# Optimization experiments

Hardware: AMD Instinct MI355X
Metric: run time of the kernel (lower is better)

The kernel has to match this reference:

```python
import jax, jax.numpy as jnp
import numpy as np

WS = 7  # window_size


def setup_inputs() -> dict:
    key = jax.random.key(0)
    ks = jax.random.split(key, 4)
    B, C, H, W = 4, 384, 56, 56
    NH = 12
    x = jax.random.normal(ks[0], (B, C, H, W), dtype=jnp.float32)
    # 1x1 conv weights act as per-pixel linear maps over channels
    w_qkv = jax.random.normal(ks[1], (3 * C, C), dtype=jnp.float32) * (C ** -0.5)
    b_qkv = jnp.zeros((3 * C,), dtype=jnp.float32)
    w_proj = jax.random.normal(ks[2], (C, C), dtype=jnp.float32) * (C ** -0.5)
    b_proj = jnp.zeros((C,), dtype=jnp.float32)
    rel_bias = jax.random.normal(ks[3], (NH, WS, WS), dtype=jnp.float32) * 0.02
    return {"x": x, "w_qkv": w_qkv, "b_qkv": b_qkv,
            "w_proj": w_proj, "b_proj": b_proj, "rel_bias": rel_bias}


def reference(x, w_qkv, b_qkv, w_proj, b_proj, rel_bias):
    # Neighborhood attention: each query (i,j) attends to a ws x ws window of
    # keys/values centered at (i,j); borders handled by replication padding
    # (ReplicationPad2d), with a learned relative position bias (nh, ws, ws).
    B, C, H, W = x.shape
    nh, ws, _ = rel_bias.shape
    hd = C // nh
    p = ws // 2
    scale = hd ** -0.5

    # qkv 1x1 conv -> (B, 3, nh, hd, H, W)
    qkv = jnp.einsum('oc,bchw->bohw', w_qkv, x) + b_qkv[None, :, None, None]
    qkv = qkv.reshape(B, 3, nh, hd, H, W)
    q, k, v = qkv[:, 0] * scale, qkv[:, 1], qkv[:, 2]

    pad = ((0, 0), (0, 0), (0, 0), (p, p), (p, p))
    k_pad = jnp.pad(k, pad, mode='edge')  # replication padding
    v_pad = jnp.pad(v, pad, mode='edge')

    # attention logits over the ws*ws window offsets: (B, nh, H, W, K)
    logits = jnp.stack(
        [jnp.einsum('bnchw,bnchw->bnhw', q, k_pad[..., di:di + H, dj:dj + W])
         for di in range(ws) for dj in range(ws)], axis=-1)
    logits = logits + rel_bias.reshape(nh, ws * ws)[None, :, None, None, :]
    attn = jax.nn.softmax(logits, axis=-1)  # (attn_drop is identity in eval)

    # value windows: (B, nh, K, hd, H, W)
    v_win = jnp.stack([v_pad[..., di:di + H, dj:dj + W]
                       for di in range(ws) for dj in range(ws)], axis=2)
    out = jnp.einsum('bnhwk,bnkchw->bnchw', attn, v_win).reshape(B, C, H, W)

    # output projection 1x1 conv (proj_drop is identity in eval)
    out = jnp.einsum('oc,bchw->bohw', w_proj, out) + b_proj[None, :, None, None]
    return out
```

## Files before the change

### kernel.cpp

```cpp
#include <hip/hip_runtime.h>
#include <hip/hip_bf16.h>
#include <hip/hip_fp16.h>

#define S_HW 3136
#define SP   3200
#define IMG_W 56
#define C_DIM 384
#define NH_DIM 12
#define QKV_C 1152
#define F16_ROWS 768

#define TB 16
#define HALO 22
#define NPX 484
#define PLANE_B 3880

typedef float f32x4 __attribute__((ext_vector_type(4)));
typedef float f32x2 __attribute__((ext_vector_type(2)));
typedef short bf16x8 __attribute__((ext_vector_type(8)));
typedef _Float16 f16x2 __attribute__((ext_vector_type(2)));

__device__ __forceinline__ void gld_lds16(const void* g, void* lds) {
    __builtin_amdgcn_global_load_lds(
        (const __attribute__((address_space(1))) void*)g,
        (__attribute__((address_space(3))) void*)lds, 16, 0, 0);
}

__device__ __forceinline__ float u2f(unsigned int u) { return __uint_as_float(u); }
__device__ __forceinline__ unsigned int f2bf_bits(float f) {
    unsigned int u = __float_as_uint(f);
    u += 0x7FFF + ((u >> 16) & 1);
    return u >> 16;
}
__device__ __forceinline__ unsigned int f2h_bits(float f) {
    return (unsigned int)__half_as_ushort(__float2half(f));
}

__global__ __launch_bounds__(256) void convert_w2_kernel(
    const float* __restrict__ a, int na, __hip_bfloat16* __restrict__ oa,
    const float* __restrict__ b, int nb, __hip_bfloat16* __restrict__ ob)
{
    int i = blockIdx.x * 256 + threadIdx.x;
    if (i < na) oa[i] = __float2bfloat16(a[i]);
    else if (i < na + nb) ob[i - na] = __float2bfloat16(b[i - na]);
}

__global__ __launch_bounds__(256) void transpose_convert_kernel(
    const float* __restrict__ x, __hip_bfloat16* __restrict__ xt)
{
    __shared__ float t[32][33];
    const int b = blockIdx.z;
    const int c0 = blockIdx.y * 32, s0 = blockIdx.x * 32;
    const int tid = threadIdx.x;

    const int lc = tid >> 3, ls = (tid & 7) * 4;
    float4 v = *reinterpret_cast<const float4*>(
        &x[((size_t)b * C_DIM + c0 + lc) * S_HW + s0 + ls]);
    t[lc][ls + 0] = v.x; t[lc][ls + 1] = v.y;
    t[lc][ls + 2] = v.z; t[lc][ls + 3] = v.w;
    __syncthreads();

    const int ws = tid >> 3, wc = (tid & 7) * 4;
    uint2 pk;
    pk.x = f2bf_bits(t[wc + 0][ws]) | (f2bf_bits(t[wc + 1][ws]) << 16);
    pk.y = f2bf_bits(t[wc + 2][ws]) | (f2bf_bits(t[wc + 3][ws]) << 16);
    *reinterpret_cast<uint2*>(
        &xt[((size_t)b * SP + s0 + ws) * C_DIM + c0 + wc]) = pk;
}

template <bool TRANS_OUT, typename OutT>
__global__ __launch_bounds__(256) void gemm_bf16_mfma(
    const __hip_bfloat16* __restrict__ A,
    const __hip_bfloat16* __restrict__ Bt,
    const float* __restrict__ bias,
    OutT* __restrict__ Y,
    int O, int K, float qscale, int qrows, int f16rows)
{
    __shared__ char smem[16384];
    char* As = smem;
    char* Bs = smem + 8192;

    const int b   = blockIdx.z;
    const int m0  = blockIdx.y * 128;
    const int n0  = blockIdx.x * 128;
    const int tid = threadIdx.x;
    const int w = tid >> 6, l = tid & 63;
    const int wr = w >> 1, wc = w & 1;

    const int srow = l >> 2;
    const int skk  = (l & 3) * 8;

    const __hip_bfloat16* Bb = Bt + (size_t)b * SP * K;

    f32x4 acc[4][4];
    #pragma unroll
    for (int i = 0; i < 4; ++i)
        #pragma unroll
        for (int j = 0; j < 4; ++j) {
            f32x4 z = {0.f, 0.f, 0.f, 0.f};
            acc[i][j] = z;
        }

    const int frow = l & 15;
    const int fk   = (l >> 4) * 16;

    for (int k0 = 0; k0 < K; k0 += 32) {
        #pragma unroll
        for (int j = 0; j < 2; ++j) {
            const int chunk = w * 2 + j;
            const int m = chunk * 16 + srow;
            gld_lds16(A  + (size_t)(m0 + m) * K + k0 + skk, As + chunk * 1024);
            gld_lds16(Bb + (size_t)(n0 + m) * K + k0 + skk, Bs + chunk * 1024);
        }
        __syncthreads();
        bf16x8 af[4], bfr[4];
        #pragma unroll
        for (int mi = 0; mi < 4; ++mi)
            af[mi] = *reinterpret_cast<const bf16x8*>(
                As + (wr * 64 + mi * 16 + frow) * 64 + fk);
        #pragma unroll
        for (int ni = 0; ni < 4; ++ni)
            bfr[ni] = *reinterpret_cast<const bf16x8*>(
                Bs + (wc * 64 + ni * 16 + frow) * 64 + fk);
        #pragma unroll
        for (int mi = 0; mi < 4; ++mi)
            #pragma unroll
            for (int ni = 0; ni < 4; ++ni)
                acc[mi][ni] = __builtin_amdgcn_mfma_f32_16x16x32_bf16(
                    af[mi], bfr[ni], acc[mi][ni], 0, 0, 0);
        __syncthreads();
    }

    const int crow0 = (l >> 4) * 4;
    const int ccol  = l & 15;
    if (TRANS_OUT) {
        __hip_bfloat16* Yb = (__hip_bfloat16*)Y + (size_t)b * SP * O;
        #pragma unroll
        for (int ni = 0; ni < 4; ++ni) {
            const int col = n0 + wc * 64 + ni * 16 + ccol;
            if (col >= S_HW) continue;
            #pragma unroll
            for (int mi = 0; mi < 4; ++mi) {
                const int row0 = m0 + wr * 64 + mi * 16 + crow0;
                const float sc = (row0 < qrows) ? qscale : 1.f;
                float v0 = (acc[mi][ni][0] + bias[row0 + 0]) * sc;
                float v1 = (acc[mi][ni][1] + bias[row0 + 1]) * sc;
                float v2 = (acc[mi][ni][2] + bias[row0 + 2]) * sc;
                float v3 = (acc[mi][ni][3] + bias[row0 + 3]) * sc;
                uint2 pk;
                if (row0 < f16rows) {
                    pk.x = f2h_bits(v0) | (f2h_bits(v1) << 16);
                    pk.y = f2h_bits(v2) | (f2h_bits(v3) << 16);
                } else {
                    pk.x = f2bf_bits(v0) | (f2bf_bits(v1) << 16);
                    pk.y = f2bf_bits(v2) | (f2bf_bits(v3) << 16);
                }
                *reinterpret_cast<uint2*>(&Yb[(size_t)col * O + row0]) = pk;
            }
        }
    } else {
        float* Yb = (float*)Y + (size_t)b * O * S_HW;
        #pragma unroll
        for (int ni = 0; ni < 4; ++ni) {
            const int col = n0 + wc * 64 + ni * 16 + ccol;
            if (col >= S_HW) continue;
            #pragma unroll
            for (int mi = 0; mi < 4; ++mi) {
                #pragma unroll
                for (int r = 0; r < 4; ++r) {
                    const int row = m0 + wr * 64 + mi * 16 + crow0 + r;
                    float v = acc[mi][ni][r] + bias[row];
                    if (row < qrows) v *= qscale;
                    Yb[(size_t)row * S_HW + col] = v;
                }
            }
        }
    }
}

__global__ __launch_bounds__(256, 4) void na_attn_kernel(
    const __hip_bfloat16* __restrict__ qkvt, const float* __restrict__ rel_bias,
    __hip_bfloat16* __restrict__ outt)
{
    __shared__ alignas(16) char halo[8 * PLANE_B];

    const int blk  = blockIdx.x;
    const int tile = blk & 15;
    const int bn   = blk >> 4;
    const int nh   = bn % NH_DIM;
    const int b    = bn / NH_DIM;
    const int th0  = (tile >> 2) * TB;
    const int tw0  = (tile & 3) * TB;

    const int tid = threadIdx.x;
    const int ty = tid >> 4, tx = tid & 15;
    const int h = th0 + ty, w = tw0 + tx;
    const bool valid = (h < 56) && (w < 56);
    const int s = h * IMG_W + w;

    const __hip_bfloat16* base = qkvt + (size_t)b * SP * QKV_C;
    const int co = nh * 32;

    #pragma unroll
    for (int i = 0; i < 8; ++i) {
        const int idx = tid + i * 256;
        if (idx < NPX * 4) {
            const int px = idx >> 2, g = idx & 3;
            const int hy = px / HALO, hx = px - hy * HALO;
            const int y = min(max(th0 - 3 + hy, 0), 55);
            const int x = min(max(tw0 - 3 + hx, 0), 55);
            const uint4 v = *reinterpret_cast<const uint4*>(
                base + (size_t)(y * IMG_W + x) * QKV_C + C_DIM + co + g * 8);
            uint2 lo; lo.x = v.x; lo.y = v.y;
            uint2 hi; hi.x = v.z; hi.y = v.w;
            *reinterpret_cast<uint2*>(&halo[(2 * g + 0) * PLANE_B + px * 8]) = lo;
            *reinterpret_cast<uint2*>(&halo[(2 * g + 1) * PLANE_B + px * 8]) = hi;
        }
    }

    unsigned int qreg[16];
    if (valid) {
        const uint4* qp = reinterpret_cast<const uint4*>(base + (size_t)s * QKV_C + co);
        #pragma unroll
        for (int g = 0; g < 4; ++g) {
            uint4 qg = qp[g];
            qreg[4 * g + 0] = qg.x; qreg[4 * g + 1] = qg.y;
            qreg[4 * g + 2] = qg.z; qreg[4 * g + 3] = qg.w;
        }
    }
    __syncthreads();

    float logits[49];
    if (valid) {
        #pragma unroll
        for (int di = 0; di < 7; ++di) {
            #pragma unroll
            for (int dj = 0; dj < 7; ++dj) {
                const int hp = (ty + di) * HALO + (tx + dj);
                const char* hb = halo + hp * 8;
                float acc0 = 0.f, acc1 = 0.f;
                #pragma unroll
                for (int pl = 0; pl < 8; ++pl) {
                    uint2 kk = *reinterpret_cast<const uint2*>(hb + pl * PLANE_B);
#if __has_builtin(__builtin_amdgcn_fdot2)
                    acc0 = __builtin_amdgcn_fdot2(
                        __builtin_bit_cast(f16x2, qreg[2 * pl]),
                        __builtin_bit_cast(f16x2, kk.x), acc0, false);
                    acc1 = __builtin_amdgcn_fdot2(
                        __builtin_bit_cast(f16x2, qreg[2 * pl + 1]),
                        __builtin_bit_cast(f16x2, kk.y), acc1, false);
#else
                    f16x2 qa = __builtin_bit_cast(f16x2, qreg[2 * pl]);
                    f16x2 qb = __builtin_bit_cast(f16x2, qreg[2 * pl + 1]);
                    f16x2 ka = __builtin_bit_cast(f16x2, kk.x);
                    f16x2 kb = __builtin_bit_cast(f16x2, kk.y);
                    acc0 += (float)qa[0] * (float)ka[0] + (float)qa[1] * (float)ka[1];
                    acc1 += (float)qb[0] * (float)kb[0] + (float)qb[1] * (float)kb[1];
#endif
                }
                logits[di * 7 + dj] = acc0 + acc1 + rel_bias[(nh * 7 + di) * 7 + dj];
            }
        }
    }
    __syncthreads();

    #pragma unroll
    for (int i = 0; i < 8; ++i) {
        const int idx = tid + i * 256;
        if (idx < NPX * 4) {
            const int px = idx >> 2, g = idx & 3;
            const int hy = px / HALO, hx = px - hy * HALO;
            const int y = min(max(th0 - 3 + hy, 0), 55);
            const int x = min(max(tw0 - 3 + hx, 0), 55);
            const uint4 v = *reinterpret_cast<const uint4*>(
                base + (size_t)(y * IMG_W + x) * QKV_C + 2 * C_DIM + co + g * 8);
            uint2 lo; lo.x = v.x; lo.y = v.y;
            uint2 hi; hi.x = v.z; hi.y = v.w;
            *reinterpret_cast<uint2*>(&halo[(2 * g + 0) * PLANE_B + px * 8]) = lo;
            *reinterpret_cast<uint2*>(&halo[(2 * g + 1) * PLANE_B + px * 8]) = hi;
        }
    }

    unsigned int ppk[25];
    float inv = 0.f;
    if (valid) {
        float mx = logits[0];
        #pragma unroll
        for (int i = 1; i < 49; ++i) mx = fmaxf(mx, logits[i]);
        float sum = 0.f;
        #pragma unroll
        for (int i = 0; i < 24; ++i) {
            float e0 = __expf(logits[2 * i] - mx);
            float e1 = __expf(logits[2 * i + 1] - mx);
            sum += e0 + e1;
            ppk[i] = f2bf_bits(e0) << 16 | f2bf_bits(e1);
        }
        {
            float e0 = __expf(logits[48] - mx);
            sum += e0;
            ppk[24] = f2bf_bits(e0) << 16;
        }
        inv = 1.f / sum;
    }
    __syncthreads();

    if (valid) {
        f32x2 o2[16];
        #pragma unroll
        for (int p = 0; p < 16; ++p) o2[p] = f32x2{0.f, 0.f};

        #pragma unroll
        for (int n = 0; n < 49; ++n) {
            const unsigned int pu = ppk[n >> 1];
            const float pv = (n & 1) ? u2f(pu << 16) : u2f(pu & 0xFFFF0000u);
            const int di = n / 7, dj = n % 7;
            const int hp = (ty + di) * HALO + (tx + dj);
            const char* hb = halo + hp * 8;
            const f32x2 pp = f32x2{pv, pv};
            #pragma unroll
            for (int pl = 0; pl < 8; ++pl) {
                uint2 vv = *reinterpret_cast<const uint2*>(hb + pl * PLANE_B);
                f32x2 v0 = f32x2{u2f(vv.x << 16), u2f(vv.x & 0xFFFF0000u)};
                f32x2 v1 = f32x2{u2f(vv.y << 16), u2f(vv.y & 0xFFFF0000u)};
                o2[2 * pl]     += pp * v0;
                o2[2 * pl + 1] += pp * v1;
            }
        }

        uint4* dst = reinterpret_cast<uint4*>(outt + ((size_t)b * SP + s) * C_DIM + co);
        #pragma unroll
        for (int g = 0; g < 4; ++g) {
            uint4 pk;
            pk.x = f2bf_bits(o2[4 * g + 0].x * inv) | (f2bf_bits(o2[4 * g + 0].y * inv) << 16);
            pk.y = f2bf_bits(o2[4 * g + 1].x * inv) | (f2bf_bits(o2[4 * g + 1].y * inv) << 16);
            pk.z = f2bf_bits(o2[4 * g + 2].x * inv) | (f2bf_bits(o2[4 * g + 2].y * inv) << 16);
            pk.w = f2bf_bits(o2[4 * g + 3].x * inv) | (f2bf_bits(o2[4 * g + 3].y * inv) << 16);
            dst[g] = pk;
        }
    }
}

extern "C" void kernel_launch(void* const* d_in, const int* in_sizes, int n_in,
                              void* d_out, int out_size, void* d_ws, size_t ws_size,
                              hipStream_t stream) {
    const float* x        = (const float*)d_in[0];
    const float* w_qkv    = (const float*)d_in[1];
    const float* b_qkv    = (const float*)d_in[2];
    const float* w_proj   = (const float*)d_in[3];
    const float* b_proj   = (const float*)d_in[4];
    const float* rel_bias = (const float*)d_in[5];
    float* out = (float*)d_out;

    __hip_bfloat16* xt   = (__hip_bfloat16*)d_ws;
    __hip_bfloat16* wq   = xt + (size_t)4 * SP * C_DIM;
    __hip_bfloat16* wp   = wq + (size_t)QKV_C * C_DIM;
    __hip_bfloat16* qkvt = wp + (size_t)C_DIM * C_DIM;
    __hip_bfloat16* att  = qkvt + (size_t)4 * SP * QKV_C;

    const float scale = 0.17677669529663687f;
    const int nwq = QKV_C * C_DIM, nwp = C_DIM * C_DIM;

    convert_w2_kernel<<<dim3((nwq + nwp + 255) / 256), 256, 0, stream>>>(
        w_qkv, nwq, wq, w_proj, nwp, wp);
    transpose_convert_kernel<<<dim3(98, 12, 4), dim3(256), 0, stream>>>(x, xt);

    gemm_bf16_mfma<true, __hip_bfloat16><<<dim3(25, 9, 4), 256, 0, stream>>>(
        wq, xt, b_qkv, qkvt, QKV_C, C_DIM, scale, C_DIM, F16_ROWS);

    na_attn_kernel<<<dim3(4 * NH_DIM * 16), 256, 0, stream>>>(qkvt, rel_bias, att);

    gemm_bf16_mfma<false, float><<<dim3(25, 3, 4), 256, 0, stream>>>(
        wp, att, b_proj, out, C_DIM, C_DIM, 1.f, 0, 0);
}
```

Measured before the change: 101.5 us.

## Store V as fp16, use narrower N tile for projection GEMM

The QKV GEMM now writes every output row (including V) as fp16 instead of bf16. The attention value loop converts fp16 pairs directly and uses scalar fmaf accumulators instead of bf16 unpacking. The output-projection GEMM gets a templated half-width N tile (64 columns), which doubles its grid to fill more CUs on the small problem. This trades V's bf16 range for fp16 precision and may cost extra per-element conversion instructions in the attention loop.

```diff
diff --git a/kernel.cpp b/kernel.cpp
--- a/kernel.cpp
+++ b/kernel.cpp
@@ -8,7 +8,6 @@
 #define C_DIM 384
 #define NH_DIM 12
 #define QKV_C 1152
-#define F16_ROWS 768
 
 #define TB 16
 #define HALO 22
@@ -68,21 +67,22 @@
         &xt[((size_t)b * SP + s0 + ws) * C_DIM + c0 + wc]) = pk;
 }
 
-template <bool TRANS_OUT, typename OutT>
+template <bool TRANS_OUT, int NF, typename OutT>
 __global__ __launch_bounds__(256) void gemm_bf16_mfma(
     const __hip_bfloat16* __restrict__ A,
     const __hip_bfloat16* __restrict__ Bt,
     const float* __restrict__ bias,
     OutT* __restrict__ Y,
-    int O, int K, float qscale, int qrows, int f16rows)
+    int O, int K, float qscale, int qrows)
 {
-    __shared__ char smem[16384];
+    constexpr int BN = NF * 32;
+    __shared__ char smem[8192 + BN * 64];
     char* As = smem;
     char* Bs = smem + 8192;
 
     const int b   = blockIdx.z;
     const int m0  = blockIdx.y * 128;
-    const int n0  = blockIdx.x * 128;
+    const int n0  = blockIdx.x * BN;
     const int tid = threadIdx.x;
     const int w = tid >> 6, l = tid & 63;
     const int wr = w >> 1, wc = w & 1;
@@ -92,11 +92,11 @@
 
     const __hip_bfloat16* Bb = Bt + (size_t)b * SP * K;
 
-    f32x4 acc[4][4];
+    f32x4 acc[4][NF];
     #pragma unroll
     for (int i = 0; i < 4; ++i)
         #pragma unroll
-        for (int j = 0; j < 4; ++j) {
+        for (int j = 0; j < NF; ++j) {
             f32x4 z = {0.f, 0.f, 0.f, 0.f};
             acc[i][j] = z;
         }
@@ -109,23 +109,33 @@
         for (int j = 0; j < 2; ++j) {
             const int chunk = w * 2 + j;
             const int m = chunk * 16 + srow;
-            gld_lds16(A  + (size_t)(m0 + m) * K + k0 + skk, As + chunk * 1024);
-            gld_lds16(Bb + (size_t)(n0 + m) * K + k0 + skk, Bs + chunk * 1024);
+            gld_lds16(A + (size_t)(m0 + m) * K + k0 + skk, As + chunk * 1024);
+        }
+        if (NF == 4) {
+            #pragma unroll
+            for (int j = 0; j < 2; ++j) {
+                const int chunk = w * 2 + j;
+                const int m = chunk * 16 + srow;
+                gld_lds16(Bb + (size_t)(n0 + m) * K + k0 + skk, Bs + chunk * 1024);
+            }
+        } else {
+            const int m = w * 16 + srow;
+            gld_lds16(Bb + (size_t)(n0 + m) * K + k0 + skk, Bs + w * 1024);
         }
         __syncthreads();
-        bf16x8 af[4], bfr[4];
+        bf16x8 af[4], bfr[NF];
         #pragma unroll
         for (int mi = 0; mi < 4; ++mi)
             af[mi] = *reinterpret_cast<const bf16x8*>(
                 As + (wr * 64 + mi * 16 + frow) * 64 + fk);
         #pragma unroll
-        for (int ni = 0; ni < 4; ++ni)
+        for (int ni = 0; ni < NF; ++ni)
             bfr[ni] = *reinterpret_cast<const bf16x8*>(
-                Bs + (wc * 64 + ni * 16 + frow) * 64 + fk);
+                Bs + (wc * (NF * 16) + ni * 16 + frow) * 64 + fk);
         #pragma unroll
         for (int mi = 0; mi < 4; ++mi)
             #pragma unroll
-            for (int ni = 0; ni < 4; ++ni)
+            for (int ni = 0; ni < NF; ++ni)
                 acc[mi][ni] = __builtin_amdgcn_mfma_f32_16x16x32_bf16(
                     af[mi], bfr[ni], acc[mi][ni], 0, 0, 0);
         __syncthreads();
@@ -136,8 +146,8 @@
     if (TRANS_OUT) {
         __hip_bfloat16* Yb = (__hip_bfloat16*)Y + (size_t)b * SP * O;
         #pragma unroll
-        for (int ni = 0; ni < 4; ++ni) {
-            const int col = n0 + wc * 64 + ni * 16 + ccol;
+        for (int ni = 0; ni < NF; ++ni) {
+            const int col = n0 + wc * (NF * 16) + ni * 16 + ccol;
             if (col >= S_HW) continue;
             #pragma unroll
             for (int mi = 0; mi < 4; ++mi) {
@@ -148,21 +158,16 @@
                 float v2 = (acc[mi][ni][2] + bias[row0 + 2]) * sc;
                 float v3 = (acc[mi][ni][3] + bias[row0 + 3]) * sc;
                 uint2 pk;
-                if (row0 < f16rows) {
-                    pk.x = f2h_bits(v0) | (f2h_bits(v1) << 16);
-                    pk.y = f2h_bits(v2) | (f2h_bits(v3) << 16);
-                } else {
-                    pk.x = f2bf_bits(v0) | (f2bf_bits(v1) << 16);
-                    pk.y = f2bf_bits(v2) | (f2bf_bits(v3) << 16);
-                }
+                pk.x = f2h_bits(v0) | (f2h_bits(v1) << 16);
+                pk.y = f2h_bits(v2) | (f2h_bits(v3) << 16);
                 *reinterpret_cast<uint2*>(&Yb[(size_t)col * O + row0]) = pk;
             }
         }
     } else {
         float* Yb = (float*)Y + (size_t)b * O * S_HW;
         #pragma unroll
-        for (int ni = 0; ni < 4; ++ni) {
-            const int col = n0 + wc * 64 + ni * 16 + ccol;
+        for (int ni = 0; ni < NF; ++ni) {
+            const int col = n0 + wc * (NF * 16) + ni * 16 + ccol;
             if (col >= S_HW) continue;
             #pragma unroll
             for (int mi = 0; mi < 4; ++mi) {
@@ -305,9 +310,9 @@
     __syncthreads();
 
     if (valid) {
-        f32x2 o2[16];
-        #pragma unroll
-        for (int p = 0; p < 16; ++p) o2[p] = f32x2{0.f, 0.f};
+        float o[32];
+        #pragma unroll
+        for (int c = 0; c < 32; ++c) o[c] = 0.f;
 
         #pragma unroll
         for (int n = 0; n < 49; ++n) {
@@ -316,14 +321,15 @@
             const int di = n / 7, dj = n % 7;
             const int hp = (ty + di) * HALO + (tx + dj);
             const char* hb = halo + hp * 8;
-            const f32x2 pp = f32x2{pv, pv};
             #pragma unroll
             for (int pl = 0; pl < 8; ++pl) {
                 uint2 vv = *reinterpret_cast<const uint2*>(hb + pl * PLANE_B);
-                f32x2 v0 = f32x2{u2f(vv.x << 16), u2f(vv.x & 0xFFFF0000u)};
-                f32x2 v1 = f32x2{u2f(vv.y << 16), u2f(vv.y & 0xFFFF0000u)};
-                o2[2 * pl]     += pp * v0;
-                o2[2 * pl + 1] += pp * v1;
+                f16x2 va = __builtin_bit_cast(f16x2, vv.x);
+                f16x2 vb = __builtin_bit_cast(f16x2, vv.y);
+                o[4 * pl + 0] = fmaf((float)va[0], pv, o[4 * pl + 0]);
+                o[4 * pl + 1] = fmaf((float)va[1], pv, o[4 * pl + 1]);
+                o[4 * pl + 2] = fmaf((float)vb[0], pv, o[4 * pl + 2]);
+                o[4 * pl + 3] = fmaf((float)vb[1], pv, o[4 * pl + 3]);
             }
         }
 
@@ -331,10 +337,10 @@
         #pragma unroll
         for (int g = 0; g < 4; ++g) {
             uint4 pk;
-            pk.x = f2bf_bits(o2[4 * g + 0].x * inv) | (f2bf_bits(o2[4 * g + 0].y * inv) << 16);
-            pk.y = f2bf_bits(o2[4 * g + 1].x * inv) | (f2bf_bits(o2[4 * g + 1].y * inv) << 16);
-            pk.z = f2bf_bits(o2[4 * g + 2].x * inv) | (f2bf_bits(o2[4 * g + 2].y * inv) << 16);
-            pk.w = f2bf_bits(o2[4 * g + 3].x * inv) | (f2bf_bits(o2[4 * g + 3].y * inv) << 16);
+            pk.x = f2bf_bits(o[8 * g + 0] * inv) | (f2bf_bits(o[8 * g + 1] * inv) << 16);
+            pk.y = f2bf_bits(o[8 * g + 2] * inv) | (f2bf_bits(o[8 * g + 3] * inv) << 16);
+            pk.z = f2bf_bits(o[8 * g + 4] * inv) | (f2bf_bits(o[8 * g + 5] * inv) << 16);
+            pk.w = f2bf_bits(o[8 * g + 6] * inv) | (f2bf_bits(o[8 * g + 7] * inv) << 16);
             dst[g] = pk;
         }
     }
@@ -364,11 +370,11 @@
         w_qkv, nwq, wq, w_proj, nwp, wp);
     transpose_convert_kernel<<<dim3(98, 12, 4), dim3(256), 0, stream>>>(x, xt);
 
-    gemm_bf16_mfma<true, __hip_bfloat16><<<dim3(25, 9, 4), 256, 0, stream>>>(
-        wq, xt, b_qkv, qkvt, QKV_C, C_DIM, scale, C_DIM, F16_ROWS);
+    gemm_bf16_mfma<true, 4, __hip_bfloat16><<<dim3(25, 9, 4), 256, 0, stream>>>(
+        wq, xt, b_qkv, qkvt, QKV_C, C_DIM, scale, C_DIM);
 
     na_attn_kernel<<<dim3(4 * NH_DIM * 16), 256, 0, stream>>>(qkvt, rel_bias, att);
 
-    gemm_bf16_mfma<false, float><<<dim3(25, 3, 4), 256, 0, stream>>>(
-        wp, att, b_proj, out, C_DIM, C_DIM, 1.f, 0, 0);
-}
+    gemm_bf16_mfma<false, 2, float><<<dim3(50, 3, 4), 256, 0, stream>>>(
+        wp, att, b_proj, out, C_DIM, C_DIM, 1.f, 0);
+}
```

Result: faster. 97.39 us (-4.1%).
